# Performance work log

Hardware: AMD Instinct MI355X
Metric: run time of the kernel (lower is better)

The kernel has to match this reference:

```python
import jax, jax.numpy as jnp
import numpy as np

MAXG = 8          # max adaptive sampling grid (boxes generated so ceil(roi_size) <= 8)
SCALE = 0.125     # spatial_scale / ds (ds = 1.0)


def setup_inputs() -> dict:
    key = jax.random.key(0)
    ks = jax.random.split(key, 12)
    bs, N, ch, H, W = 8, 128, 1280, 64, 64
    out_ch, inner = 1024, 5120
    z = jax.random.normal(ks[0], (bs, ch, H, W), jnp.float32)
    # boxes (x1, y1, x2, y2) in 512x512 image coords, sizes in [8, 64] px
    x1 = jax.random.uniform(ks[1], (bs, N), minval=0.0, maxval=448.0)
    y1 = jax.random.uniform(ks[2], (bs, N), minval=0.0, maxval=448.0)
    bw = jax.random.uniform(ks[3], (bs, N), minval=8.0, maxval=64.0)
    bh = jax.random.uniform(ks[4], (bs, N), minval=8.0, maxval=64.0)
    bboxes = jnp.stack([x1, y1, x1 + bw, y1 + bh], axis=-1)

    def lin(k, fan_in, shape):
        return jax.random.normal(k, shape, jnp.float32) * (1.0 / np.sqrt(fan_in))

    W1 = lin(ks[5], ch, (ch, inner)); b1 = jnp.zeros((inner,), jnp.float32)
    W2 = lin(ks[6], inner, (inner, out_ch)); b2 = jnp.zeros((out_ch,), jnp.float32)
    S1 = lin(ks[7], 2, (2, 64)); sb1 = jnp.zeros((64,), jnp.float32)
    S2 = lin(ks[8], 64, (64, 256)); sb2 = jnp.zeros((256,), jnp.float32)
    S3 = lin(ks[9], 256, (256, out_ch)); sb3 = jnp.zeros((out_ch,), jnp.float32)
    O = lin(ks[10], 2 * out_ch, (2 * out_ch, out_ch)); ob = jnp.zeros((out_ch,), jnp.float32)
    return dict(z=z, bboxes=bboxes, W1=W1, b1=b1, W2=W2, b2=b2,
                S1=S1, sb1=sb1, S2=S2, sb2=sb2, S3=S3, sb3=sb3, O=O, ob=ob)


def _prep(c, size):
    # torchvision bilinear border handling for one coordinate axis
    oob = (c < -1.0) | (c > size)
    cc = jnp.clip(c, 0.0, None)
    lo0 = jnp.floor(cc)
    hi_case = lo0 >= size - 1
    lo = jnp.minimum(lo0, size - 1).astype(jnp.int32)
    hi = jnp.minimum(lo0 + 1, size - 1).astype(jnp.int32)
    frac = jnp.where(hi_case, 0.0, cc - lo0)
    return lo, hi, frac, oob


def _roi_align_1x1(z, bboxes):
    # torchvision roi_align, output_size=1, aligned=True, sampling_ratio=-1
    bs, ch, H, W = z.shape
    N = bboxes.shape[1]
    boxes = jax.lax.stop_gradient(bboxes).reshape(-1, 4) * SCALE - 0.5  # aligned
    bidx = jnp.repeat(jnp.arange(bs), N)
    rw = boxes[:, 2] - boxes[:, 0]
    rh = boxes[:, 3] - boxes[:, 1]
    gw = jnp.clip(jnp.ceil(rw), 1, MAXG)   # adaptive grid: ceil(roi_size / 1)
    gh = jnp.clip(jnp.ceil(rh), 1, MAXG)
    count = gh * gw
    i = jnp.arange(MAXG, dtype=jnp.float32)
    ys = boxes[:, 1:2] + (i[None] + 0.5) * rh[:, None] / gh[:, None]  # [R, G]
    xs = boxes[:, 0:1] + (i[None] + 0.5) * rw[:, None] / gw[:, None]
    vy = i[None] < gh[:, None]
    vx = i[None] < gw[:, None]
    yl, yh, fy, oy = _prep(ys, H)
    xl, xh, fx, ox = _prep(xs, W)
    my = (vy & ~oy).astype(z.dtype)
    mx = (vx & ~ox).astype(z.dtype)
    mask = my[:, :, None] * mx[:, None, :]             # [R, G, G]
    hy, ly = 1.0 - fy, fy
    hx, lx = 1.0 - fx, fx
    zt = jnp.transpose(z, (0, 2, 3, 1))                # [bs, H, W, ch]
    acc = jnp.zeros((bs * N, ch), z.dtype)
    corners = [(yl, xl, hy, hx), (yl, xh, hy, lx), (yh, xl, ly, hx), (yh, xh, ly, lx)]
    for yi, xi, wy, wx in corners:
        wt = mask * (wy[:, :, None] * wx[:, None, :])  # [R, G, G]
        v = zt[bidx[:, None, None], yi[:, :, None], xi[:, None, :]]  # [R, G, G, ch]
        acc = acc + jnp.einsum('rgh,rghc->rc', wt, v)
    return (acc / count[:, None]).reshape(bs, N, ch)


def reference(z, bboxes, W1, b1, W2, b2, S1, sb1, S2, sb2, S3, sb3, O, ob):
    x = _roi_align_1x1(z, bboxes)                      # [bs, N, ch]
    x = jax.nn.relu(x @ W1 + b1) @ W2 + b2             # out MLP
    # BBoxSizeEmbedder: (h, w) = (y2 - y1, x2 - x1)
    sz = jnp.stack([bboxes[..., 3] - bboxes[..., 1],
                    bboxes[..., 2] - bboxes[..., 0]], axis=-1)
    e = jax.nn.relu(sz @ S1 + sb1)
    e = jax.nn.relu(e @ S2 + sb2)
    e = e @ S3 + sb3
    return jnp.concatenate([x, e], axis=-1) @ O + ob   # out2
```

## Files before the change

kernel.cpp:

```cpp
#include <hip/hip_runtime.h>

static constexpr int kBS    = 8;
static constexpr int kNROI  = 128;
static constexpr int kR     = kBS * kNROI;
static constexpr int kCH    = 1280;
static constexpr int kH     = 64;
static constexpr int kW     = 64;
static constexpr int kPIX   = kH * kW;
static constexpr int kINNER = 5120;
static constexpr int kOUTC  = 1024;
static constexpr int kXE    = 2 * kOUTC;
static constexpr int kE2    = 256;

typedef _Float16 half8 __attribute__((ext_vector_type(8)));
typedef float floatx4 __attribute__((ext_vector_type(4)));

__device__ __forceinline__ void gload_lds16(const _Float16* g, _Float16* l) {
    __builtin_amdgcn_global_load_lds(
        (const __attribute__((address_space(1))) void*)g,
        (__attribute__((address_space(3))) void*)l,
        16, 0, 0);
}

__global__ __launch_bounds__(256) void transpose_z_f16(const float* __restrict__ z,
                                                       _Float16* __restrict__ zt) {
    __shared__ float tile[64][33];
    const int b  = blockIdx.z;
    const int p0 = blockIdx.x * 32;
    const int c0 = blockIdx.y * 64;
    const int tx = threadIdx.x;
    const int ty = threadIdx.y;
    const float* zb = z + (size_t)b * kCH * kPIX;
    _Float16* ztb = zt + (size_t)b * kPIX * kCH;
#pragma unroll
    for (int i = 0; i < 8; ++i) {
        const int cl = ty + i * 8;
        tile[cl][tx] = zb[(size_t)(c0 + cl) * kPIX + p0 + tx];
    }
    __syncthreads();
#pragma unroll
    for (int i = 0; i < 4; ++i) {
        const int pl = ty + i * 8;
        union { _Float16 h[2]; unsigned int u; } pk;
        pk.h[0] = (_Float16)tile[2 * tx][pl];
        pk.h[1] = (_Float16)tile[2 * tx + 1][pl];
        *(unsigned int*)(ztb + (size_t)(p0 + pl) * kCH + c0 + 2 * tx) = pk.u;
    }
}

struct RoiLists {
    int   yidx[16], xidx[16];
    float ywt[16], xwt[16];
    int   ny, nx;
    float invCount;
};

__device__ inline void build_lists(const float* __restrict__ bboxes, int r, RoiLists* L) {
    const float x1 = bboxes[r * 4 + 0] * 0.125f - 0.5f;
    const float y1 = bboxes[r * 4 + 1] * 0.125f - 0.5f;
    const float x2 = bboxes[r * 4 + 2] * 0.125f - 0.5f;
    const float y2 = bboxes[r * 4 + 3] * 0.125f - 0.5f;
    const float rw = x2 - x1, rh = y2 - y1;
    const float gwf = fminf(fmaxf(ceilf(rw), 1.0f), 8.0f);
    const float ghf = fminf(fmaxf(ceilf(rh), 1.0f), 8.0f);
    const int gw = (int)gwf, gh = (int)ghf;
    L->invCount = 1.0f / (gwf * ghf);
    for (int g = 0; g < gh; ++g) {
        const float c   = y1 + ((float)g + 0.5f) * rh / ghf;
        const bool oob  = (c < -1.0f) || (c > 64.0f);
        const float cc  = fmaxf(c, 0.0f);
        const float lo0 = floorf(cc);
        const bool hic  = (lo0 >= 63.0f);
        const int lo    = (int)fminf(lo0, 63.0f);
        const int hi    = (int)fminf(lo0 + 1.0f, 63.0f);
        const float fr  = hic ? 0.0f : (cc - lo0);
        const float m   = oob ? 0.0f : 1.0f;
        L->yidx[2 * g]     = lo; L->ywt[2 * g]     = m * (1.0f - fr);
        L->yidx[2 * g + 1] = hi; L->ywt[2 * g + 1] = m * fr;
    }
    L->ny = 2 * gh;
    for (int g = 0; g < gw; ++g) {
        const float c   = x1 + ((float)g + 0.5f) * rw / gwf;
        const bool oob  = (c < -1.0f) || (c > 64.0f);
        const float cc  = fmaxf(c, 0.0f);
        const float lo0 = floorf(cc);
        const bool hic  = (lo0 >= 63.0f);
        const int lo    = (int)fminf(lo0, 63.0f);
        const int hi    = (int)fminf(lo0 + 1.0f, 63.0f);
        const float fr  = hic ? 0.0f : (cc - lo0);
        const float m   = oob ? 0.0f : 1.0f;
        L->xidx[2 * g]     = lo; L->xwt[2 * g]     = m * (1.0f - fr);
        L->xidx[2 * g + 1] = hi; L->xwt[2 * g + 1] = m * fr;
    }
    L->nx = 2 * gw;
}

__global__ __launch_bounds__(256) void roi_gather_f16(const _Float16* __restrict__ zt,
                                                      const float* __restrict__ bboxes,
                                                      _Float16* __restrict__ x) {
    const int r = blockIdx.x;
    const int b = r >> 7;
    __shared__ RoiLists L;
    if (threadIdx.x == 0) build_lists(bboxes, r, &L);
    __syncthreads();
    const int ny = L.ny, nx = L.nx;
    const float ic = L.invCount;
    const _Float16* ztb = zt + (size_t)b * kPIX * kCH;
    for (int c8 = threadIdx.x; c8 < kCH / 8; c8 += 256) {
        float acc[8] = {0.f, 0.f, 0.f, 0.f, 0.f, 0.f, 0.f, 0.f};
        for (int iy = 0; iy < ny; ++iy) {
            const float wy = L.ywt[iy];
            const int Yb   = L.yidx[iy] * kW;
            for (int ix = 0; ix < nx; ++ix) {
                const float w = wy * L.xwt[ix];
                const half8 v = *(const half8*)(ztb + (size_t)(Yb + L.xidx[ix]) * kCH + c8 * 8);
#pragma unroll
                for (int q = 0; q < 8; ++q) acc[q] += w * (float)v[q];
            }
        }
        half8 o;
#pragma unroll
        for (int q = 0; q < 8; ++q) o[q] = (_Float16)(acc[q] * ic);
        *(half8*)&x[(size_t)r * kCH + c8 * 8] = o;
    }
}

__global__ __launch_bounds__(256) void roi_gather_direct(const float* __restrict__ z,
                                                         const float* __restrict__ bboxes,
                                                         _Float16* __restrict__ x) {
    const int r = blockIdx.x;
    const int b = r >> 7;
    __shared__ RoiLists L;
    if (threadIdx.x == 0) build_lists(bboxes, r, &L);
    __syncthreads();
    const int ny = L.ny, nx = L.nx;
    const float ic = L.invCount;
    const float* zb = z + (size_t)b * kCH * kPIX;
    for (int c = threadIdx.x; c < kCH; c += 256) {
        const float* zc = zb + (size_t)c * kPIX;
        float acc = 0.f;
        for (int iy = 0; iy < ny; ++iy) {
            const float wy = L.ywt[iy];
            const int base = L.yidx[iy] * kW;
            for (int ix = 0; ix < nx; ++ix)
                acc += wy * L.xwt[ix] * zc[base + L.xidx[ix]];
        }
        x[(size_t)r * kCH + c] = (_Float16)(acc * ic);
    }
}

__global__ __launch_bounds__(256) void convert_transpose(const float* __restrict__ W,
                                                         _Float16* __restrict__ Wt,
                                                         int K, int N) {
    __shared__ float tile[32][33];
    const int n0 = blockIdx.x * 32;
    const int k0 = blockIdx.y * 32;
    const int tx = threadIdx.x;
    const int ty = threadIdx.y;
#pragma unroll
    for (int i = 0; i < 4; ++i)
        tile[ty + i * 8][tx] = W[(size_t)(k0 + ty + i * 8) * N + n0 + tx];
    __syncthreads();
#pragma unroll
    for (int i = 0; i < 4; ++i)
        Wt[(size_t)(n0 + ty + i * 8) * K + k0 + tx] = (_Float16)tile[tx][ty + i * 8];
}

template <int NSPLIT, bool FUSED, bool RELU, bool F16OUT>
__global__ __launch_bounds__(256) void gemm_f16(const _Float16* __restrict__ A,
                                                const _Float16* __restrict__ Bt,
                                                const float* __restrict__ bias,
                                                void* __restrict__ Out,
                                                int Kfull, int ldc) {
    __shared__ _Float16 As[128 * 32];
    __shared__ _Float16 Bs[128 * 32];
    const int t    = threadIdx.x;
    const int lane = t & 63;
    const int wave = t >> 6;
    const int m0 = blockIdx.y * 128, n0 = blockIdx.x * 128;
    const int Ksplit = Kfull / NSPLIT;
    const int s  = FUSED ? 0 : blockIdx.z;
    const int Nn = gridDim.x * 128;
    const int Mm = gridDim.y * 128;

    const int c0 = t, c1 = t + 256;
    const _Float16* Ag0 = A + (size_t)(m0 + (c0 >> 2)) * Kfull + (c0 & 3) * 8 + s * Ksplit;
    const _Float16* Ag1 = A + (size_t)(m0 + (c1 >> 2)) * Kfull + (c1 & 3) * 8 + s * Ksplit;
    const _Float16* Bg0 = Bt + (size_t)(n0 + (c0 >> 2)) * Kfull + (c0 & 3) * 8 + s * Ksplit;
    const _Float16* Bg1 = Bt + (size_t)(n0 + (c1 >> 2)) * Kfull + (c1 & 3) * 8 + s * Ksplit;
    _Float16* Al0 = &As[c0 * 8];
    _Float16* Al1 = &As[c1 * 8];
    _Float16* Bl0 = &Bs[c0 * 8];
    _Float16* Bl1 = &Bs[c1 * 8];

    const int wm = (wave >> 1) * 64;
    const int wn = (wave & 1) * 64;
    const int fm = lane & 15;
    const int kq = (lane >> 4) * 8;

    floatx4 acc[4][4];
#pragma unroll
    for (int i = 0; i < 4; ++i)
#pragma unroll
        for (int j = 0; j < 4; ++j) acc[i][j] = (floatx4){0.f, 0.f, 0.f, 0.f};

    for (int k0i = 0; k0i < Ksplit; k0i += 32) {
        __syncthreads();
        gload_lds16(Ag0 + k0i, Al0);
        gload_lds16(Ag1 + k0i, Al1);
        gload_lds16(Bg0 + k0i, Bl0);
        gload_lds16(Bg1 + k0i, Bl1);
        __syncthreads();

        half8 af[4], bfv[4];
#pragma unroll
        for (int i = 0; i < 4; ++i)
            af[i] = *(const half8*)&As[(wm + i * 16 + fm) * 32 + kq];
#pragma unroll
        for (int j = 0; j < 4; ++j)
            bfv[j] = *(const half8*)&Bs[(wn + j * 16 + fm) * 32 + kq];
#pragma unroll
        for (int i = 0; i < 4; ++i)
#pragma unroll
            for (int j = 0; j < 4; ++j)
                acc[i][j] = __builtin_amdgcn_mfma_f32_16x16x32_f16(af[i], bfv[j], acc[i][j], 0, 0, 0);
    }

    const int qr = (lane >> 4) * 4;
    if (FUSED) {
#pragma unroll
        for (int j = 0; j < 4; ++j) {
            const int col = n0 + wn + j * 16 + fm;
            const float bv = bias[col];
#pragma unroll
            for (int i = 0; i < 4; ++i) {
                const int row = m0 + wm + i * 16 + qr;
#pragma unroll
                for (int rr = 0; rr < 4; ++rr) {
                    float v = acc[i][j][rr] + bv;
                    if (RELU) v = fmaxf(v, 0.f);
                    if (F16OUT)
                        ((_Float16*)Out)[(size_t)(row + rr) * ldc + col] = (_Float16)v;
                    else
                        ((float*)Out)[(size_t)(row + rr) * ldc + col] = v;
                }
            }
        }
    } else {
        float* Pp = (float*)Out + (size_t)s * Mm * Nn;
#pragma unroll
        for (int j = 0; j < 4; ++j) {
            const int col = n0 + wn + j * 16 + fm;
#pragma unroll
            for (int i = 0; i < 4; ++i) {
                const int row = m0 + wm + i * 16 + qr;
#pragma unroll
                for (int rr = 0; rr < 4; ++rr)
                    Pp[(size_t)(row + rr) * Nn + col] = acc[i][j][rr];
            }
        }
    }
}

template <bool RELU, bool F16OUT, int NSPLIT>
__global__ __launch_bounds__(256) void reduce_splitk(const float* __restrict__ P,
                                                     const float* __restrict__ bias,
                                                     void* __restrict__ Cout,
                                                     int Nn, int ldc) {
    const size_t idx = ((size_t)blockIdx.x * 256 + threadIdx.x) * 4;
    const size_t MN  = (size_t)gridDim.x * 1024;
    const int m = (int)(idx / (size_t)Nn);
    const int n = (int)(idx % (size_t)Nn);
    float4 acc = *(const float4*)(P + idx);
#pragma unroll
    for (int s = 1; s < NSPLIT; ++s) {
        const float4 v = *(const float4*)(P + (size_t)s * MN + idx);
        acc.x += v.x; acc.y += v.y; acc.z += v.z; acc.w += v.w;
    }
    const float4 b4 = *(const float4*)(bias + n);
    acc.x += b4.x; acc.y += b4.y; acc.z += b4.z; acc.w += b4.w;
    if (RELU) {
        acc.x = fmaxf(acc.x, 0.f); acc.y = fmaxf(acc.y, 0.f);
        acc.z = fmaxf(acc.z, 0.f); acc.w = fmaxf(acc.w, 0.f);
    }
    if (F16OUT) {
        union { _Float16 h[4]; uint2 u; } pk;
        pk.h[0] = (_Float16)acc.x; pk.h[1] = (_Float16)acc.y;
        pk.h[2] = (_Float16)acc.z; pk.h[3] = (_Float16)acc.w;
        *(uint2*)((_Float16*)Cout + (size_t)m * ldc + n) = pk.u;
    } else {
        *(float4*)((float*)Cout + (size_t)m * ldc + n) = acc;
    }
}

__global__ __launch_bounds__(256) void size_mlp12(const float* __restrict__ bboxes,
                                                  const float* __restrict__ S1,
                                                  const float* __restrict__ sb1,
                                                  const float* __restrict__ S2,
                                                  const float* __restrict__ sb2,
                                                  _Float16* __restrict__ h2out) {
    const int r0 = blockIdx.x * 4;
    const int t  = threadIdx.x;
    __shared__ float sz[4][2];
    __shared__ float h1[4][64];
    if (t < 8) {
        const int row = t >> 1;
        const int c   = t & 1;
        const float* bb = bboxes + (size_t)(r0 + row) * 4;
        sz[row][c] = (c == 0) ? (bb[3] - bb[1]) : (bb[2] - bb[0]);
    }
    __syncthreads();
    {
        const int row = t >> 6;
        const int j   = t & 63;
        const float v = sz[row][0] * S1[j] + sz[row][1] * S1[64 + j] + sb1[j];
        h1[row][j] = fmaxf(v, 0.0f);
    }
    __syncthreads();
    {
        float acc[4];
        const float b = sb2[t];
#pragma unroll
        for (int row = 0; row < 4; ++row) acc[row] = b;
#pragma unroll 16
        for (int k = 0; k < 64; ++k) {
            const float w = S2[k * 256 + t];
#pragma unroll
            for (int row = 0; row < 4; ++row) acc[row] += h1[row][k] * w;
        }
#pragma unroll
        for (int row = 0; row < 4; ++row)
            h2out[(size_t)(r0 + row) * kE2 + t] = (_Float16)fmaxf(acc[row], 0.0f);
    }
}

extern "C" void kernel_launch(void* const* d_in, const int* in_sizes, int n_in,
                              void* d_out, int out_size, void* d_ws, size_t ws_size,
                              hipStream_t stream) {
    (void)in_sizes; (void)n_in; (void)out_size;
    const float* z   = (const float*)d_in[0];
    const float* bb  = (const float*)d_in[1];
    const float* W1  = (const float*)d_in[2];
    const float* b1  = (const float*)d_in[3];
    const float* W2  = (const float*)d_in[4];
    const float* b2  = (const float*)d_in[5];
    const float* S1  = (const float*)d_in[6];
    const float* sb1 = (const float*)d_in[7];
    const float* S2  = (const float*)d_in[8];
    const float* sb2 = (const float*)d_in[9];
    const float* S3  = (const float*)d_in[10];
    const float* sb3 = (const float*)d_in[11];
    const float* O   = (const float*)d_in[12];
    const float* ob  = (const float*)d_in[13];
    float* out = (float*)d_out;

    char* ws = (char*)d_ws;
    size_t off = 0;
    auto alloc = [&](size_t bytes) {
        void* p = ws + off;
        off += (bytes + 255) & ~(size_t)255;
        return p;
    };
    _Float16* x    = (_Float16*)alloc((size_t)kR * kCH * 2);
    _Float16* h    = (_Float16*)alloc((size_t)kR * kINNER * 2);
    _Float16* xe   = (_Float16*)alloc((size_t)kR * kXE * 2);
    _Float16* W1t  = (_Float16*)alloc((size_t)kINNER * kCH * 2);
    _Float16* W2t  = (_Float16*)alloc((size_t)kOUTC * kINNER * 2);
    _Float16* Ot   = (_Float16*)alloc((size_t)kOUTC * kXE * 2);
    _Float16* S3t  = (_Float16*)alloc((size_t)kOUTC * kE2 * 2);
    _Float16* h2f  = (_Float16*)alloc((size_t)kR * kE2 * 2);
    float*    P    = (float*)alloc((size_t)4 * kR * kOUTC * 4);
    const size_t ztBytes = (size_t)kBS * kPIX * kCH * 2;
    _Float16* zt  = (_Float16*)(ws + off);
    const bool useT = (off + ztBytes) <= ws_size;

    hipLaunchKernelGGL(convert_transpose, dim3(kINNER / 32, kCH / 32), dim3(32, 8), 0, stream,
                       W1, W1t, kCH, kINNER);
    hipLaunchKernelGGL(convert_transpose, dim3(kOUTC / 32, kINNER / 32), dim3(32, 8), 0, stream,
                       W2, W2t, kINNER, kOUTC);
    hipLaunchKernelGGL(convert_transpose, dim3(kOUTC / 32, kXE / 32), dim3(32, 8), 0, stream,
                       O, Ot, kXE, kOUTC);
    hipLaunchKernelGGL(convert_transpose, dim3(kOUTC / 32, kE2 / 32), dim3(32, 8), 0, stream,
                       S3, S3t, kE2, kOUTC);

    if (useT) {
        hipLaunchKernelGGL(transpose_z_f16, dim3(kPIX / 32, kCH / 64, kBS), dim3(32, 8), 0,
                           stream, z, zt);
        hipLaunchKernelGGL(roi_gather_f16, dim3(kR), dim3(256), 0, stream, zt, bb, x);
    } else {
        hipLaunchKernelGGL(roi_gather_direct, dim3(kR), dim3(256), 0, stream, z, bb, x);
    }

    hipLaunchKernelGGL(size_mlp12, dim3(kR / 4), dim3(256), 0, stream,
                       bb, S1, sb1, S2, sb2, h2f);
    hipLaunchKernelGGL((gemm_f16<1, true, false, true>),
                       dim3(kOUTC / 128, kR / 128, 1), dim3(256), 0, stream,
                       h2f, S3t, sb3, xe + kOUTC, kE2, kXE);

    hipLaunchKernelGGL((gemm_f16<1, true, true, true>),
                       dim3(kINNER / 128, kR / 128, 1), dim3(256), 0, stream,
                       x, W1t, b1, h, kCH, kINNER);

    hipLaunchKernelGGL((gemm_f16<4, false, false, false>),
                       dim3(kOUTC / 128, kR / 128, 4), dim3(256), 0, stream,
                       h, W2t, nullptr, P, kINNER, 0);
    hipLaunchKernelGGL((reduce_splitk<false, true, 4>),
                       dim3((size_t)kR * kOUTC / 1024), dim3(256), 0, stream,
                       P, b2, xe, kOUTC, kXE);

    hipLaunchKernelGGL((gemm_f16<4, false, false, false>),
                       dim3(kOUTC / 128, kR / 128, 4), dim3(256), 0, stream,
                       xe, Ot, nullptr, P, kXE, 0);
    hipLaunchKernelGGL((reduce_splitk<false, false, 4>),
                       dim3((size_t)kR * kOUTC / 1024), dim3(256), 0, stream,
                       P, ob, out, kOUTC, kOUTC);
}
```

Baseline: 471.2 us.

## Double-buffer GEMM LDS, split-K small GEMMs, and parallelize ROI gather over channels

```diff
diff --git a/kernel.cpp b/kernel.cpp
--- a/kernel.cpp
+++ b/kernel.cpp
@@ -95,34 +95,45 @@
     L->nx = 2 * gw;
 }
 
-__global__ __launch_bounds__(256) void roi_gather_f16(const _Float16* __restrict__ zt,
-                                                      const float* __restrict__ bboxes,
-                                                      _Float16* __restrict__ x) {
-    const int r = blockIdx.x;
-    const int b = r >> 7;
+__global__ __launch_bounds__(256) void roi_gather_f16_v2(const _Float16* __restrict__ zt,
+                                                         const float* __restrict__ bboxes,
+                                                         _Float16* __restrict__ x) {
+    const int r  = blockIdx.y;
+    const int b  = r >> 7;
+    const int cg = blockIdx.x * 32;
+    const int t  = threadIdx.x;
     __shared__ RoiLists L;
-    if (threadIdx.x == 0) build_lists(bboxes, r, &L);
-    __syncthreads();
-    const int ny = L.ny, nx = L.nx;
-    const float ic = L.invCount;
-    const _Float16* ztb = zt + (size_t)b * kPIX * kCH;
-    for (int c8 = threadIdx.x; c8 < kCH / 8; c8 += 256) {
-        float acc[8] = {0.f, 0.f, 0.f, 0.f, 0.f, 0.f, 0.f, 0.f};
-        for (int iy = 0; iy < ny; ++iy) {
-            const float wy = L.ywt[iy];
-            const int Yb   = L.yidx[iy] * kW;
-            for (int ix = 0; ix < nx; ++ix) {
-                const float w = wy * L.xwt[ix];
-                const half8 v = *(const half8*)(ztb + (size_t)(Yb + L.xidx[ix]) * kCH + c8 * 8);
-#pragma unroll
-                for (int q = 0; q < 8; ++q) acc[q] += w * (float)v[q];
-            }
-        }
-        half8 o;
-#pragma unroll
-        for (int q = 0; q < 8; ++q) o[q] = (_Float16)(acc[q] * ic);
-        *(half8*)&x[(size_t)r * kCH + c8 * 8] = o;
-    }
+    __shared__ int   off[256];
+    __shared__ float wt[256];
+    __shared__ float accs[8][32][9];
+    if (t == 0) build_lists(bboxes, r, &L);
+    __syncthreads();
+    const int np = L.ny * L.nx;
+    if (t < np) {
+        const int iy = t / L.nx;
+        const int ix = t - iy * L.nx;
+        off[t] = (L.yidx[iy] * kW + L.xidx[ix]) * kCH;
+        wt[t]  = L.ywt[iy] * L.xwt[ix];
+    }
+    __syncthreads();
+    const int lc = t & 31;
+    const int pg = t >> 5;
+    const _Float16* base = zt + (size_t)b * kPIX * kCH + (size_t)(cg + lc) * 8;
+    float a[8] = {0.f, 0.f, 0.f, 0.f, 0.f, 0.f, 0.f, 0.f};
+    for (int p = pg; p < np; p += 8) {
+        const float w = wt[p];
+        const half8 v = *(const half8*)(base + off[p]);
+#pragma unroll
+        for (int q = 0; q < 8; ++q) a[q] += w * (float)v[q];
+    }
+#pragma unroll
+    for (int q = 0; q < 8; ++q) accs[pg][lc][q] = a[q];
+    __syncthreads();
+    const int rc = t >> 3, ch = t & 7;
+    float s = 0.f;
+#pragma unroll
+    for (int g = 0; g < 8; ++g) s += accs[g][rc][ch];
+    x[(size_t)r * kCH + (size_t)(cg + rc) * 8 + ch] = (_Float16)(s * L.invCount);
 }
 
 __global__ __launch_bounds__(256) void roi_gather_direct(const float* __restrict__ z,
@@ -172,8 +183,8 @@
                                                 const float* __restrict__ bias,
                                                 void* __restrict__ Out,
                                                 int Kfull, int ldc) {
-    __shared__ _Float16 As[128 * 32];
-    __shared__ _Float16 Bs[128 * 32];
+    __shared__ _Float16 As[2][128 * 32];
+    __shared__ _Float16 Bs[2][128 * 32];
     const int t    = threadIdx.x;
     const int lane = t & 63;
     const int wave = t >> 6;
@@ -188,10 +199,6 @@
     const _Float16* Ag1 = A + (size_t)(m0 + (c1 >> 2)) * Kfull + (c1 & 3) * 8 + s * Ksplit;
     const _Float16* Bg0 = Bt + (size_t)(n0 + (c0 >> 2)) * Kfull + (c0 & 3) * 8 + s * Ksplit;
     const _Float16* Bg1 = Bt + (size_t)(n0 + (c1 >> 2)) * Kfull + (c1 & 3) * 8 + s * Ksplit;
-    _Float16* Al0 = &As[c0 * 8];
-    _Float16* Al1 = &As[c1 * 8];
-    _Float16* Bl0 = &Bs[c0 * 8];
-    _Float16* Bl1 = &Bs[c1 * 8];
 
     const int wm = (wave >> 1) * 64;
     const int wn = (wave & 1) * 64;
@@ -204,26 +211,36 @@
 #pragma unroll
         for (int j = 0; j < 4; ++j) acc[i][j] = (floatx4){0.f, 0.f, 0.f, 0.f};
 
-    for (int k0i = 0; k0i < Ksplit; k0i += 32) {
-        __syncthreads();
-        gload_lds16(Ag0 + k0i, Al0);
-        gload_lds16(Ag1 + k0i, Al1);
-        gload_lds16(Bg0 + k0i, Bl0);
-        gload_lds16(Bg1 + k0i, Bl1);
-        __syncthreads();
-
+    const int nsteps = Ksplit / 32;
+
+    gload_lds16(Ag0, &As[0][c0 * 8]);
+    gload_lds16(Ag1, &As[0][c1 * 8]);
+    gload_lds16(Bg0, &Bs[0][c0 * 8]);
+    gload_lds16(Bg1, &Bs[0][c1 * 8]);
+    __syncthreads();
+
+    for (int ks = 0; ks < nsteps; ++ks) {
+        const int cur = ks & 1;
+        if (ks + 1 < nsteps) {
+            const int kn = (ks + 1) * 32;
+            gload_lds16(Ag0 + kn, &As[cur ^ 1][c0 * 8]);
+            gload_lds16(Ag1 + kn, &As[cur ^ 1][c1 * 8]);
+            gload_lds16(Bg0 + kn, &Bs[cur ^ 1][c0 * 8]);
+            gload_lds16(Bg1 + kn, &Bs[cur ^ 1][c1 * 8]);
+        }
         half8 af[4], bfv[4];
 #pragma unroll
         for (int i = 0; i < 4; ++i)
-            af[i] = *(const half8*)&As[(wm + i * 16 + fm) * 32 + kq];
+            af[i] = *(const half8*)&As[cur][(wm + i * 16 + fm) * 32 + kq];
 #pragma unroll
         for (int j = 0; j < 4; ++j)
-            bfv[j] = *(const half8*)&Bs[(wn + j * 16 + fm) * 32 + kq];
+            bfv[j] = *(const half8*)&Bs[cur][(wn + j * 16 + fm) * 32 + kq];
 #pragma unroll
         for (int i = 0; i < 4; ++i)
 #pragma unroll
             for (int j = 0; j < 4; ++j)
                 acc[i][j] = __builtin_amdgcn_mfma_f32_16x16x32_f16(af[i], bfv[j], acc[i][j], 0, 0, 0);
+        __syncthreads();
     }
 
     const int qr = (lane >> 4) * 4;
@@ -369,7 +386,7 @@
     _Float16* Ot   = (_Float16*)alloc((size_t)kOUTC * kXE * 2);
     _Float16* S3t  = (_Float16*)alloc((size_t)kOUTC * kE2 * 2);
     _Float16* h2f  = (_Float16*)alloc((size_t)kR * kE2 * 2);
-    float*    P    = (float*)alloc((size_t)4 * kR * kOUTC * 4);
+    float*    P    = (float*)alloc((size_t)2 * kR * kINNER * 4);
     const size_t ztBytes = (size_t)kBS * kPIX * kCH * 2;
     _Float16* zt  = (_Float16*)(ws + off);
     const bool useT = (off + ztBytes) <= ws_size;
@@ -386,20 +403,27 @@
     if (useT) {
         hipLaunchKernelGGL(transpose_z_f16, dim3(kPIX / 32, kCH / 64, kBS), dim3(32, 8), 0,
                            stream, z, zt);
-        hipLaunchKernelGGL(roi_gather_f16, dim3(kR), dim3(256), 0, stream, zt, bb, x);
+        hipLaunchKernelGGL(roi_gather_f16_v2, dim3(kCH / 256, kR), dim3(256), 0, stream,
+                           zt, bb, x);
     } else {
         hipLaunchKernelGGL(roi_gather_direct, dim3(kR), dim3(256), 0, stream, z, bb, x);
     }
 
     hipLaunchKernelGGL(size_mlp12, dim3(kR / 4), dim3(256), 0, stream,
                        bb, S1, sb1, S2, sb2, h2f);
-    hipLaunchKernelGGL((gemm_f16<1, true, false, true>),
-                       dim3(kOUTC / 128, kR / 128, 1), dim3(256), 0, stream,
-                       h2f, S3t, sb3, xe + kOUTC, kE2, kXE);
-
-    hipLaunchKernelGGL((gemm_f16<1, true, true, true>),
-                       dim3(kINNER / 128, kR / 128, 1), dim3(256), 0, stream,
-                       x, W1t, b1, h, kCH, kINNER);
+    hipLaunchKernelGGL((gemm_f16<4, false, false, false>),
+                       dim3(kOUTC / 128, kR / 128, 4), dim3(256), 0, stream,
+                       h2f, S3t, nullptr, P, kE2, 0);
+    hipLaunchKernelGGL((reduce_splitk<false, true, 4>),
+                       dim3((size_t)kR * kOUTC / 1024), dim3(256), 0, stream,
+                       P, sb3, xe + kOUTC, kOUTC, kXE);
+
+    hipLaunchKernelGGL((gemm_f16<2, false, false, false>),
+                       dim3(kINNER / 128, kR / 128, 2), dim3(256), 0, stream,
+                       x, W1t, nullptr, P, kCH, 0);
+    hipLaunchKernelGGL((reduce_splitk<true, true, 2>),
+                       dim3((size_t)kR * kINNER / 1024), dim3(256), 0, stream,
+                       P, b1, h, kINNER, kINNER);
 
     hipLaunchKernelGGL((gemm_f16<4, false, false, false>),
                        dim3(kOUTC / 128, kR / 128, 4), dim3(256), 0, stream,
```

Result: faster. 458.8 us (-2.6%).
